# Performance work log

Hardware: AMD Instinct MI355X
Metric: run time of the kernel (lower is better)

## Reference

```python
import jax, jax.numpy as jnp
import numpy as np

B, N, M = 8, 1_000_000, 1_000


def setup_inputs() -> dict:
    key = jax.random.key(0)
    k1, k2, k3 = jax.random.split(key, 3)
    # vertices: positions (3) + normals (3) per vertex
    batch_vertices = jax.random.normal(k1, (B, N, 6), dtype=jnp.float32)
    # triangle indices (unused by this forward, kept for interface fidelity)
    batch_indices = jax.random.randint(k2, (B, M, 3), 0, N)
    # well-conditioned affine transforms: top 3x4 = [I + 0.1*randn | t], bottom row [0,0,0,1]
    top = jax.random.normal(k3, (B, 3, 4), dtype=jnp.float32) * 0.1
    top = top.at[:, :, :3].add(jnp.eye(3, dtype=jnp.float32))
    bottom = jnp.broadcast_to(jnp.array([0.0, 0.0, 0.0, 1.0], dtype=jnp.float32), (B, 1, 4))
    batch_transforms = jnp.concatenate([top, bottom], axis=1)  # (B, 4, 4)
    return {
        "batch_vertices": batch_vertices,
        "batch_indices": batch_indices,
        "batch_transforms": batch_transforms,
    }


def reference(batch_vertices, batch_indices, batch_transforms):
    # batch_vertices: (B, N, 6); batch_transforms: (B, 4, 4)
    pos = batch_vertices[..., :3]
    ones = jnp.ones(pos.shape[:-1] + (1,), dtype=pos.dtype)
    homog = jnp.concatenate([pos, ones], axis=-1)            # (B, N, 4)
    # transformed = homog @ T^T  (per mesh)
    t = jnp.einsum("bnj,bij->bni", homog, batch_transforms)  # (B, N, 4)
    new_pos = t[..., :3] / t[..., 3:4]
    # normals: rotate by 3x3 block, renormalize
    nrm = batch_vertices[..., 3:6]
    R = batch_transforms[:, :3, :3]
    tn = jnp.einsum("bnj,bij->bni", nrm, R)                  # (B, N, 3)
    ln = jnp.maximum(jnp.linalg.norm(tn, axis=-1, keepdims=True), 1e-8)
    new_nrm = tn / ln
    return jnp.concatenate([new_pos, new_nrm], axis=-1)      # (B, N, 6)
```

## Files before the change

### kernel.cpp

```cpp
#include <hip/hip_runtime.h>


constexpr int TPB     = 256;
constexpr int F4PT    = 3;
constexpr int TILE_F4 = TPB * F4PT;

__global__ __launch_bounds__(TPB)
void GPUBatchProcessor_68186900791881_kernel(const float4* __restrict__ vin,
                                             const float* __restrict__ xf,
                                             float4* __restrict__ vout,
                                             int f4_per_batch,
                                             int pairs_per_batch)
{
    __shared__ float4 lds[TILE_F4];
    const int t = threadIdx.x;
    const int b = blockIdx.y;
    const long long batchBase = (long long)b * f4_per_batch;
    const int tileF4 = blockIdx.x * TILE_F4;

    const float4* src = vin + batchBase;
#pragma unroll
    for (int k = 0; k < F4PT; ++k) {
        int f = tileF4 + k * TPB + t;
        if (f < f4_per_batch) lds[k * TPB + t] = src[f];
    }
    __syncthreads();

    const float4* T = reinterpret_cast<const float4*>(xf) + (size_t)b * 4;
    const float4 r0 = T[0], r1 = T[1], r2 = T[2], r3 = T[3];

    const int p = blockIdx.x * TPB + t;
    if (p < pairs_per_batch) {
        const float4 q0 = lds[t * 3 + 0];
        const float4 q1 = lds[t * 3 + 1];
        const float4 q2 = lds[t * 3 + 2];

        float o[12];
#pragma unroll
        for (int v = 0; v < 2; ++v) {
            float px, py, pz, nx, ny, nz;
            if (v == 0) { px = q0.x; py = q0.y; pz = q0.z; nx = q0.w; ny = q1.x; nz = q1.y; }
            else        { px = q1.z; py = q1.w; pz = q2.x; nx = q2.y; ny = q2.z; nz = q2.w; }

            float tx = r0.x * px + r0.y * py + r0.z * pz + r0.w;
            float ty = r1.x * px + r1.y * py + r1.z * pz + r1.w;
            float tz = r2.x * px + r2.y * py + r2.z * pz + r2.w;
            float tw = r3.x * px + r3.y * py + r3.z * pz + r3.w;
            float invw = 1.0f / tw;
            tx *= invw; ty *= invw; tz *= invw;

            float mx = r0.x * nx + r0.y * ny + r0.z * nz;
            float my = r1.x * nx + r1.y * ny + r1.z * nz;
            float mz = r2.x * nx + r2.y * ny + r2.z * nz;
            float len = fmaxf(sqrtf(mx * mx + my * my + mz * mz), 1e-8f);
            float inv = 1.0f / len;
            mx *= inv; my *= inv; mz *= inv;

            o[v * 6 + 0] = tx; o[v * 6 + 1] = ty; o[v * 6 + 2] = tz;
            o[v * 6 + 3] = mx; o[v * 6 + 4] = my; o[v * 6 + 5] = mz;
        }

        lds[t * 3 + 0] = make_float4(o[0], o[1], o[2],  o[3]);
        lds[t * 3 + 1] = make_float4(o[4], o[5], o[6],  o[7]);
        lds[t * 3 + 2] = make_float4(o[8], o[9], o[10], o[11]);
    }
    __syncthreads();

    float4* dst = vout + batchBase;
#pragma unroll
    for (int k = 0; k < F4PT; ++k) {
        int f = tileF4 + k * TPB + t;
        if (f < f4_per_batch) dst[f] = lds[k * TPB + t];
    }
}

extern "C" void kernel_launch(void* const* d_in, const int* in_sizes, int n_in,
                              void* d_out, int out_size, void* d_ws, size_t ws_size,
                              hipStream_t stream) {
    const float* verts = (const float*)d_in[0];
    const float* xf    = (const float*)d_in[2];
    float*       out   = (float*)d_out;

    const int B = in_sizes[2] / 16;
    const long long totalV = (long long)in_sizes[0] / 6;
    const int N = (int)(totalV / B);
    const int f4_per_batch   = N * 6 / 4;
    const int pairs_per_batch = N / 2;

    const int tiles = (f4_per_batch + TILE_F4 - 1) / TILE_F4;
    dim3 grid(tiles, B);
    GPUBatchProcessor_68186900791881_kernel<<<grid, TPB, 0, stream>>>(
        reinterpret_cast<const float4*>(verts), xf,
        reinterpret_cast<float4*>(out), f4_per_batch, pairs_per_batch);
}
```

Measured before the change: 74.58 us.

## Double-buffer tiles with async global-to-LDS loads across persistent blocks

```diff
diff --git a/kernel.cpp b/kernel.cpp
--- a/kernel.cpp
+++ b/kernel.cpp
@@ -4,73 +4,133 @@
 constexpr int TPB     = 256;
 constexpr int F4PT    = 3;
 constexpr int TILE_F4 = TPB * F4PT;
+constexpr int TPBLK   = 9;
+
+typedef const __attribute__((address_space(1))) void* gp_t;
+typedef __attribute__((address_space(3))) void*       lp_t;
+typedef float __attribute__((ext_vector_type(4)))     f32x4;
+
+__device__ __forceinline__ void xform_pair(const float4& r0, const float4& r1,
+                                           const float4& r2, const float4& r3,
+                                           float4& q0, float4& q1, float4& q2)
+{
+    float o[12];
+#pragma unroll
+    for (int v = 0; v < 2; ++v) {
+        float px, py, pz, nx, ny, nz;
+        if (v == 0) { px = q0.x; py = q0.y; pz = q0.z; nx = q0.w; ny = q1.x; nz = q1.y; }
+        else        { px = q1.z; py = q1.w; pz = q2.x; nx = q2.y; ny = q2.z; nz = q2.w; }
+        float tx = r0.x*px + r0.y*py + r0.z*pz + r0.w;
+        float ty = r1.x*px + r1.y*py + r1.z*pz + r1.w;
+        float tz = r2.x*px + r2.y*py + r2.z*pz + r2.w;
+        float tw = r3.x*px + r3.y*py + r3.z*pz + r3.w;
+        float invw = 1.0f / tw;
+        tx *= invw; ty *= invw; tz *= invw;
+        float mx = r0.x*nx + r0.y*ny + r0.z*nz;
+        float my = r1.x*nx + r1.y*ny + r1.z*nz;
+        float mz = r2.x*nx + r2.y*ny + r2.z*nz;
+        float len = fmaxf(sqrtf(mx*mx + my*my + mz*mz), 1e-8f);
+        float inv = 1.0f / len;
+        mx *= inv; my *= inv; mz *= inv;
+        o[v*6+0] = tx; o[v*6+1] = ty; o[v*6+2] = tz;
+        o[v*6+3] = mx; o[v*6+4] = my; o[v*6+5] = mz;
+    }
+    q0 = make_float4(o[0], o[1], o[2],  o[3]);
+    q1 = make_float4(o[4], o[5], o[6],  o[7]);
+    q2 = make_float4(o[8], o[9], o[10], o[11]);
+}
 
 __global__ __launch_bounds__(TPB)
 void GPUBatchProcessor_68186900791881_kernel(const float4* __restrict__ vin,
                                              const float* __restrict__ xf,
                                              float4* __restrict__ vout,
                                              int f4_per_batch,
-                                             int pairs_per_batch)
+                                             int pipe_blocks)
 {
-    __shared__ float4 lds[TILE_F4];
+    __shared__ float4 lds[2][TILE_F4];
     const int t = threadIdx.x;
     const int b = blockIdx.y;
     const long long batchBase = (long long)b * f4_per_batch;
-    const int tileF4 = blockIdx.x * TILE_F4;
+    const float4* src = vin + batchBase;
+    float4*       dst = vout + batchBase;
 
-    const float4* src = vin + batchBase;
+    const float4* T4 = reinterpret_cast<const float4*>(xf) + (size_t)b * 4;
+    const float4 r0 = T4[0], r1 = T4[1], r2 = T4[2], r3 = T4[3];
+
+    if (blockIdx.x < pipe_blocks) {
+        const long long tile0 = (long long)blockIdx.x * TPBLK;
+        {
+            const float4* s = src + tile0 * TILE_F4;
 #pragma unroll
-    for (int k = 0; k < F4PT; ++k) {
-        int f = tileF4 + k * TPB + t;
-        if (f < f4_per_batch) lds[k * TPB + t] = src[f];
-    }
-    __syncthreads();
+            for (int k = 0; k < F4PT; ++k)
+                __builtin_amdgcn_global_load_lds((gp_t)(s + k*TPB + t),
+                                                 (lp_t)&lds[0][k*TPB + t], 16, 0, 0);
+        }
+#pragma unroll
+        for (int i = 0; i < TPBLK; ++i) {
+            const int cur = i & 1;
+            if (i + 1 < TPBLK) {
+                const float4* s = src + (tile0 + i + 1) * TILE_F4;
+#pragma unroll
+                for (int k = 0; k < F4PT; ++k)
+                    __builtin_amdgcn_global_load_lds((gp_t)(s + k*TPB + t),
+                                                     (lp_t)&lds[cur ^ 1][k*TPB + t], 16, 0, 0);
+            }
+            if (i == 0 || i + 1 == TPBLK) asm volatile("s_waitcnt vmcnt(3)" ::: "memory");
+            else                          asm volatile("s_waitcnt vmcnt(6)" ::: "memory");
+            __builtin_amdgcn_s_barrier();
+            __builtin_amdgcn_sched_barrier(0);
 
-    const float4* T = reinterpret_cast<const float4*>(xf) + (size_t)b * 4;
-    const float4 r0 = T[0], r1 = T[1], r2 = T[2], r3 = T[3];
+            float4 q0 = lds[cur][t*3 + 0];
+            float4 q1 = lds[cur][t*3 + 1];
+            float4 q2 = lds[cur][t*3 + 2];
+            xform_pair(r0, r1, r2, r3, q0, q1, q2);
+            lds[cur][t*3 + 0] = q0;
+            lds[cur][t*3 + 1] = q1;
+            lds[cur][t*3 + 2] = q2;
 
-    const int p = blockIdx.x * TPB + t;
-    if (p < pairs_per_batch) {
-        const float4 q0 = lds[t * 3 + 0];
-        const float4 q1 = lds[t * 3 + 1];
-        const float4 q2 = lds[t * 3 + 2];
+            asm volatile("s_waitcnt lgkmcnt(0)" ::: "memory");
+            __builtin_amdgcn_s_barrier();
+            __builtin_amdgcn_sched_barrier(0);
 
-        float o[12];
+            const long long tb = (tile0 + i) * TILE_F4;
+            const f32x4* l = reinterpret_cast<const f32x4*>(&lds[cur][0]);
+            f32x4* d = reinterpret_cast<f32x4*>(dst + tb);
 #pragma unroll
-        for (int v = 0; v < 2; ++v) {
-            float px, py, pz, nx, ny, nz;
-            if (v == 0) { px = q0.x; py = q0.y; pz = q0.z; nx = q0.w; ny = q1.x; nz = q1.y; }
-            else        { px = q1.z; py = q1.w; pz = q2.x; nx = q2.y; ny = q2.z; nz = q2.w; }
-
-            float tx = r0.x * px + r0.y * py + r0.z * pz + r0.w;
-            float ty = r1.x * px + r1.y * py + r1.z * pz + r1.w;
-            float tz = r2.x * px + r2.y * py + r2.z * pz + r2.w;
-            float tw = r3.x * px + r3.y * py + r3.z * pz + r3.w;
-            float invw = 1.0f / tw;
-            tx *= invw; ty *= invw; tz *= invw;
-
-            float mx = r0.x * nx + r0.y * ny + r0.z * nz;
-            float my = r1.x * nx + r1.y * ny + r1.z * nz;
-            float mz = r2.x * nx + r2.y * ny + r2.z * nz;
-            float len = fmaxf(sqrtf(mx * mx + my * my + mz * mz), 1e-8f);
-            float inv = 1.0f / len;
-            mx *= inv; my *= inv; mz *= inv;
-
-            o[v * 6 + 0] = tx; o[v * 6 + 1] = ty; o[v * 6 + 2] = tz;
-            o[v * 6 + 3] = mx; o[v * 6 + 4] = my; o[v * 6 + 5] = mz;
+            for (int k = 0; k < F4PT; ++k)
+                __builtin_nontemporal_store(l[k*TPB + t], d + k*TPB + t);
         }
-
-        lds[t * 3 + 0] = make_float4(o[0], o[1], o[2],  o[3]);
-        lds[t * 3 + 1] = make_float4(o[4], o[5], o[6],  o[7]);
-        lds[t * 3 + 2] = make_float4(o[8], o[9], o[10], o[11]);
-    }
-    __syncthreads();
-
-    float4* dst = vout + batchBase;
+    } else {
+        const long long tailStart = (long long)pipe_blocks * TPBLK * TILE_F4;
+        const int nTail = gridDim.x - pipe_blocks;
+        for (long long base = tailStart + (long long)(blockIdx.x - pipe_blocks) * TILE_F4;
+             base < f4_per_batch;
+             base += (long long)nTail * TILE_F4) {
+            int rem = (int)(f4_per_batch - base); if (rem > TILE_F4) rem = TILE_F4;
+            __syncthreads();
 #pragma unroll
-    for (int k = 0; k < F4PT; ++k) {
-        int f = tileF4 + k * TPB + t;
-        if (f < f4_per_batch) dst[f] = lds[k * TPB + t];
+            for (int k = 0; k < F4PT; ++k) {
+                int f = k*TPB + t;
+                if (f < rem) lds[0][f] = src[base + f];
+            }
+            __syncthreads();
+            const int npairs = rem / F4PT;
+            if (t < npairs) {
+                float4 q0 = lds[0][t*3 + 0];
+                float4 q1 = lds[0][t*3 + 1];
+                float4 q2 = lds[0][t*3 + 2];
+                xform_pair(r0, r1, r2, r3, q0, q1, q2);
+                lds[0][t*3 + 0] = q0;
+                lds[0][t*3 + 1] = q1;
+                lds[0][t*3 + 2] = q2;
+            }
+            __syncthreads();
+#pragma unroll
+            for (int k = 0; k < F4PT; ++k) {
+                int f = k*TPB + t;
+                if (f < rem) dst[base + f] = lds[0][f];
+            }
+        }
     }
 }
 
@@ -84,12 +144,13 @@
     const int B = in_sizes[2] / 16;
     const long long totalV = (long long)in_sizes[0] / 6;
     const int N = (int)(totalV / B);
-    const int f4_per_batch   = N * 6 / 4;
-    const int pairs_per_batch = N / 2;
+    const int f4_per_batch = N * 6 / 4;
 
-    const int tiles = (f4_per_batch + TILE_F4 - 1) / TILE_F4;
-    dim3 grid(tiles, B);
+    const int full_tiles  = f4_per_batch / TILE_F4;
+    const int pipe_blocks = full_tiles / TPBLK;
+
+    dim3 grid(pipe_blocks + 1, B);
     GPUBatchProcessor_68186900791881_kernel<<<grid, TPB, 0, stream>>>(
         reinterpret_cast<const float4*>(verts), xf,
-        reinterpret_cast<float4*>(out), f4_per_batch, pairs_per_batch);
+        reinterpret_cast<float4*>(out), f4_per_batch, pipe_blocks);
 }
```

After: 63.61 us. -14.7%, faster.
